# Performance work log

Measured on AMD Instinct MI355X. Metric: run time of the kernel, lower is better.

Reference implementation:

```python
import jax, jax.numpy as jnp
import numpy as np

NUM_EMBEDDINGS = 1024
EMBEDDING_DIM = 256
COMMITMENT_COST = 0.25


def setup_inputs() -> dict:
    key = jax.random.key(0)
    k1, k2 = jax.random.split(key)
    inputs = jax.random.normal(k1, (32, EMBEDDING_DIM, 32, 32), dtype=jnp.float32)
    # codebook init matches torch: uniform(-1/K, 1/K)
    weight = jax.random.uniform(
        k2, (NUM_EMBEDDINGS, EMBEDDING_DIM), dtype=jnp.float32,
        minval=-1.0 / NUM_EMBEDDINGS, maxval=1.0 / NUM_EMBEDDINGS)
    return {"inputs": inputs, "weight": weight}


def reference(inputs, weight):
    # inputs: [B, C, H, W] with C == EMBEDDING_DIM; weight: [K, D]
    x = jnp.transpose(inputs, (0, 2, 3, 1))            # [B, H, W, D]
    input_shape = x.shape
    flat = x.reshape(-1, EMBEDDING_DIM)                # [N, D]

    distances = (jnp.sum(flat * flat, axis=1, keepdims=True)
                 + jnp.sum(weight * weight, axis=1)
                 - 2.0 * (flat @ weight.T))
    encoding_indices = jnp.argmin(distances, axis=1)   # [N]
    encodings = jax.nn.one_hot(encoding_indices, NUM_EMBEDDINGS, dtype=jnp.float32)  # [N, K]

    # one_hot @ weight == gather; use gather for efficiency (same values)
    quantized = weight[encoding_indices].reshape(input_shape)  # [B, H, W, D]

    e_latent_loss = jnp.mean((jax.lax.stop_gradient(quantized) - x) ** 2)
    q_latent_loss = jnp.mean((quantized - jax.lax.stop_gradient(x)) ** 2)
    loss = q_latent_loss + COMMITMENT_COST * e_latent_loss

    # straight-through estimator
    quantized_st = x + jax.lax.stop_gradient(quantized - x)

    avg_probs = jnp.mean(encodings, axis=0)            # [K]
    perplexity = jnp.exp(-jnp.sum(avg_probs * jnp.log(avg_probs + 1e-10)))

    return (loss,
            jnp.transpose(quantized_st, (0, 3, 1, 2)),  # back to [B, C, H, W]
            perplexity,
            encodings)
```

## Files before the change

### kernel.cpp

```cpp
#include <hip/hip_runtime.h>
#include <hip/hip_bf16.h>

#define HWDIM 1024
#define DDIM 256
#define KCODES 1024
#define NROWS 32768
#define BSTRIDE (DDIM * HWDIM)
#define GUARD 1.5e-4f

typedef __attribute__((ext_vector_type(8))) short short8;
typedef __attribute__((ext_vector_type(4))) float f32x4;
typedef unsigned long long ull;


__device__ __forceinline__ unsigned short f2bf(float v) {
  __hip_bfloat16 b = __float2bfloat16(v);
  return *reinterpret_cast<unsigned short*>(&b);
}
__device__ __forceinline__ float bf2f(unsigned short u) {
  __hip_bfloat16 b;
  *reinterpret_cast<unsigned short*>(&b) = u;
  return __bfloat162float(b);
}
__device__ __forceinline__ ull pk(float d, int k) {
  unsigned ub = __float_as_uint(d);
  ub = (ub & 0x80000000u) ? ~ub : (ub | 0x80000000u);
  return ((ull)ub << 32) | (unsigned)k;
}
__device__ __forceinline__ float keyq(ull key) {
  unsigned ub = (unsigned)(key >> 32);
  unsigned orig = (ub & 0x80000000u) ? (ub & 0x7FFFFFFFu) : ~ub;
  return __uint_as_float(orig);
}

__device__ __forceinline__ float pair128_sq(const float* p, int stride) {
  float a[8];
#pragma unroll
  for (int j = 0; j < 8; ++j) { float v = p[j * stride]; a[j] = __fmul_rn(v, v); }
  for (int i = 8; i < 128; i += 8) {
#pragma unroll
    for (int j = 0; j < 8; ++j) {
      float v = p[(i + j) * stride];
      a[j] = __fadd_rn(a[j], __fmul_rn(v, v));
    }
  }
  float s01 = __fadd_rn(a[0], a[1]), s23 = __fadd_rn(a[2], a[3]);
  float s45 = __fadd_rn(a[4], a[5]), s67 = __fadd_rn(a[6], a[7]);
  return __fadd_rn(__fadd_rn(s01, s23), __fadd_rn(s45, s67));
}

__global__ __launch_bounds__(256) void k_prep(
    const float* __restrict__ w, float* __restrict__ wT, float* __restrict__ ss,
    int* __restrict__ hist, double* __restrict__ loss, int* __restrict__ wcount,
    unsigned short* __restrict__ wh8, unsigned short* __restrict__ wl8) {
  __shared__ float tile[64][65];
  const int t = threadIdx.x;
  int g = blockIdx.x * 256 + t;
  {
    int k = g >> 5, oct = g & 31;
    const float* p = w + k * DDIM + oct * 8;
    short8 hv, lv;
#pragma unroll
    for (int j = 0; j < 8; ++j) {
      float v = p[j];
      unsigned short h = f2bf(v);
      unsigned short l = f2bf(__fsub_rn(v, bf2f(h)));
      hv[j] = (short)h; lv[j] = (short)l;
    }
    *(short8*)&wh8[oct * 8192 + k * 8] = hv;
    *(short8*)&wl8[oct * 8192 + k * 8] = lv;
  }
  if (g < KCODES) {
    hist[g] = 0;
    const float* p = w + g * DDIM;
    ss[g] = __fadd_rn(pair128_sq(p, 1), pair128_sq(p + 128, 1));
  }
  if (g == 0) { *loss = 0.0; *wcount = 0; }
  if (blockIdx.x < 64) {
    const int k0 = (blockIdx.x & 15) * 64, d0 = (blockIdx.x >> 4) * 64;
    const int c = t & 63, r = t >> 6;
#pragma unroll
    for (int m = 0; m < 16; ++m)
      tile[r + m * 4][c] = w[(k0 + r + m * 4) * DDIM + d0 + c];
    __syncthreads();
#pragma unroll
    for (int m = 0; m < 16; ++m)
      wT[(size_t)(d0 + r + m * 4) * KCODES + k0 + c] = tile[c][r + m * 4];
  }
}

__global__ __launch_bounds__(256) void k_argmfma(
    const float* __restrict__ in,
    const unsigned short* __restrict__ wh8, const unsigned short* __restrict__ wl8,
    const float* __restrict__ ss, unsigned* __restrict__ kkarr,
    int* __restrict__ wlist, int* __restrict__ wcount) {
  __shared__ __align__(16) unsigned short Ah[32 * 64 * 8];
  __shared__ __align__(16) unsigned short Al[32 * 64 * 8];
  __shared__ ull best1[64], best2[64];

  const int t = threadIdx.x;
  const int n0 = blockIdx.x * 64;
  const int b = n0 >> 10, hw0 = n0 & 1023;

  {
    const int hw = t & 63, dg = t >> 6;
    const float* xp = in + b * BSTRIDE + hw0 + hw;
#pragma unroll
    for (int dd = 0; dd < 64; dd += 2) {
      int d = dg * 64 + dd;
      float f0 = xp[d * HWDIM], f1 = xp[(d + 1) * HWDIM];
      unsigned short h0 = f2bf(f0);
      unsigned short l0 = f2bf(__fsub_rn(f0, bf2f(h0)));
      unsigned short h1 = f2bf(f1);
      unsigned short l1 = f2bf(__fsub_rn(f1, bf2f(h1)));
      int base = ((d >> 3) * 64 + hw) * 8 + (d & 7);
      *(unsigned*)&Ah[base] = (unsigned)h0 | ((unsigned)h1 << 16);
      *(unsigned*)&Al[base] = (unsigned)l0 | ((unsigned)l1 << 16);
    }
  }
  if (t < 64) { best1[t] = ~0ull; best2[t] = ~0ull; }
  __syncthreads();

  const int wv = t >> 6, ln = t & 63;
  const int rw = (wv & 1) * 32;
  const int cw = (wv >> 1) * 64;
  const int l15 = ln & 15, quad = ln >> 4;

  ull rb1[8], rb2[8];
#pragma unroll
  for (int i = 0; i < 8; ++i) { rb1[i] = ~0ull; rb2[i] = ~0ull; }

  for (int kb = 0; kb < 8; ++kb) {
    const int cb = kb * 128 + cw;
    f32x4 acc[2][4];
#pragma unroll
    for (int rt = 0; rt < 2; ++rt)
#pragma unroll
      for (int ct = 0; ct < 4; ++ct) acc[rt][ct] = (f32x4){0.f, 0.f, 0.f, 0.f};

#pragma unroll
    for (int ki = 0; ki < 8; ++ki) {
      const int obase = ki * 4 + quad;
      short8 ah[2], al[2], bh[4], bl[4];
#pragma unroll
      for (int rt = 0; rt < 2; ++rt) {
        int row = rw + rt * 16 + l15;
        ah[rt] = *(const short8*)&Ah[(obase * 64 + row) * 8];
        al[rt] = *(const short8*)&Al[(obase * 64 + row) * 8];
      }
#pragma unroll
      for (int ct = 0; ct < 4; ++ct) {
        int off = obase * 8192 + (cb + ct * 16 + l15) * 8;
        bh[ct] = *(const short8*)&wh8[off];
        bl[ct] = *(const short8*)&wl8[off];
      }
#pragma unroll
      for (int rt = 0; rt < 2; ++rt)
#pragma unroll
        for (int ct = 0; ct < 4; ++ct) {
          acc[rt][ct] = __builtin_amdgcn_mfma_f32_16x16x32_bf16(ah[rt], bh[ct], acc[rt][ct], 0, 0, 0);
          acc[rt][ct] = __builtin_amdgcn_mfma_f32_16x16x32_bf16(ah[rt], bl[ct], acc[rt][ct], 0, 0, 0);
          acc[rt][ct] = __builtin_amdgcn_mfma_f32_16x16x32_bf16(al[rt], bh[ct], acc[rt][ct], 0, 0, 0);
        }
    }

    float sv[4];
#pragma unroll
    for (int ct = 0; ct < 4; ++ct) sv[ct] = ss[cb + ct * 16 + l15];
#pragma unroll
    for (int rt = 0; rt < 2; ++rt)
#pragma unroll
      for (int reg = 0; reg < 4; ++reg) {
        int idx = rt * 4 + reg;
        ull b1 = rb1[idx], b2 = rb2[idx];
#pragma unroll
        for (int ct = 0; ct < 4; ++ct) {
          float q = fmaf(-2.f, acc[rt][ct][reg], sv[ct]);
          ull key = pk(q, cb + ct * 16 + l15);
          if (key < b1) { b2 = b1; b1 = key; } else if (key < b2) { b2 = key; }
        }
        rb1[idx] = b1; rb2[idx] = b2;
      }
  }

#pragma unroll
  for (int rt = 0; rt < 2; ++rt)
#pragma unroll
    for (int reg = 0; reg < 4; ++reg)
      atomicMin(&best1[rw + rt * 16 + quad * 4 + reg], rb1[rt * 4 + reg]);
  __syncthreads();
#pragma unroll
  for (int rt = 0; rt < 2; ++rt)
#pragma unroll
    for (int reg = 0; reg < 4; ++reg) {
      int row = rw + rt * 16 + quad * 4 + reg;
      int idx = rt * 4 + reg;
      ull sub = (rb1[idx] == best1[row]) ? rb2[idx] : rb1[idx];
      atomicMin(&best2[row], sub);
    }
  __syncthreads();
  if (t < 64) {
    ull k1 = best1[t];
    kkarr[n0 + t] = (unsigned)(k1 & 0xFFFFFFFFull);
    if (!(keyq(best2[t]) - keyq(k1) > GUARD)) {
      int p = atomicAdd(wcount, 1);
      wlist[p] = n0 + t;
    }
  }
}

__global__ __launch_bounds__(256) void k_zero(float* __restrict__ e) {
  const size_t tid = (size_t)blockIdx.x * 256 + threadIdx.x;
  float4* p4 = reinterpret_cast<float4*>(e + 2);
  const float4 z = make_float4(0.f, 0.f, 0.f, 0.f);
  const size_t stride = (size_t)gridDim.x * 256;
  for (size_t i = tid; i < 8388607ull; i += stride) p4[i] = z;
  if (tid == 0) { e[0] = 0.f; e[1] = 0.f; e[33554430] = 0.f; e[33554431] = 0.f; }
}

__global__ __launch_bounds__(256) void k_fallback(
    const float* __restrict__ in, const float* __restrict__ wT,
    const float* __restrict__ ss, const int* __restrict__ wlist,
    const int* __restrict__ wcount, unsigned* __restrict__ kkarr) {
  __shared__ float xrow[256];
  __shared__ float rsh;
  __shared__ ull bmin;
  const int t = threadIdx.x;
  const int cnt = *wcount;
  for (int i = blockIdx.x; i < cnt; i += gridDim.x) {
    const int n = wlist[i];
    const int b = n >> 10, hw = n & 1023;
    xrow[t] = in[b * BSTRIDE + t * HWDIM + hw];
    if (t == 0) bmin = ~0ull;
    __syncthreads();
    if (t == 0) rsh = __fadd_rn(pair128_sq(xrow, 1), pair128_sq(xrow + 128, 1));
    __syncthreads();
    float m[4] = {0.f, 0.f, 0.f, 0.f};
    for (int d = 0; d < 256; ++d) {
      float xv = xrow[d];
      const float* wd = wT + (size_t)d * KCODES + t;
      m[0] = fmaf(xv, wd[0], m[0]);
      m[1] = fmaf(xv, wd[256], m[1]);
      m[2] = fmaf(xv, wd[512], m[2]);
      m[3] = fmaf(xv, wd[768], m[3]);
    }
    ull lb = ~0ull;
#pragma unroll
    for (int j = 0; j < 4; ++j) {
      int k = t + j * 256;
      float dist = fmaf(-2.f, m[j], __fadd_rn(rsh, ss[k]));
      ull key = pk(dist, k);
      if (key < lb) lb = key;
    }
    atomicMin(&bmin, lb);
    __syncthreads();
    if (t == 0) kkarr[n] = (unsigned)(bmin & 0xFFFFFFFFull);
    __syncthreads();
  }
}

__global__ __launch_bounds__(256) void k_quant(
    const float* __restrict__ in, const float* __restrict__ w,
    const unsigned* __restrict__ kkarr, int* __restrict__ hist,
    float* __restrict__ enc, float* __restrict__ outq, double* __restrict__ loss) {
  __shared__ float wrow[64][65];
  __shared__ unsigned kk[64];
  __shared__ double red[256];

  const int t = threadIdx.x;
  const int n0 = (blockIdx.x >> 2) * 64;
  const int dc = (blockIdx.x & 3) * 64;
  const int b = n0 >> 10, hw0 = n0 & 1023;

  if (t < 64) kk[t] = kkarr[n0 + t];
  __syncthreads();

  if (dc == 0 && t < 64) {
    unsigned k = kk[t];
    atomicAdd(&hist[k], 1);
    enc[(size_t)(n0 + t) * 1024 + k] = 1.0f;
  }

#pragma unroll
  for (int m = 0; m < 16; ++m) {
    int u = t + m * 256;
    int r = u >> 6, dd = u & 63;
    wrow[r][dd] = w[kk[r] * DDIM + dc + dd];
  }
  __syncthreads();

  const float* inb = in + b * BSTRIDE + hw0;
  float* outb = outq + b * BSTRIDE + hw0;
  const int hwl = t & 63, dl = t >> 6;
  double lsum = 0.0;
#pragma unroll
  for (int dd = 0; dd < 64; dd += 4) {
    int d = dc + dd + dl;
    float x = inb[d * HWDIM + hwl];
    float wv = wrow[hwl][dd + dl];
    float diff = __fsub_rn(wv, x);
    outb[d * HWDIM + hwl] = __fadd_rn(x, diff);
    lsum += (double)diff * (double)diff;
  }
  red[t] = lsum;
  __syncthreads();
  for (int s = 128; s > 0; s >>= 1) {
    if (t < s) red[t] += red[t + s];
    __syncthreads();
  }
  if (t == 0) atomicAdd(loss, red[0]);
}

__global__ void k_final(const int* __restrict__ hist, const double* __restrict__ loss,
                        float* __restrict__ out) {
  __shared__ double red[256];
  int t = threadIdx.x;
  double s = 0.0;
  for (int i = t; i < KCODES; i += 256) {
    double p = (double)hist[i] * (1.0 / 32768.0);
    s += p * log(p + 1e-10);
  }
  red[t] = s;
  __syncthreads();
  for (int st = 128; st > 0; st >>= 1) {
    if (t < st) red[t] += red[t + st];
    __syncthreads();
  }
  if (t == 0) {
    out[8388609] = (float)exp(-red[0]);
    double m = *loss / 8388608.0;
    out[0] = (float)(1.25 * m);
  }
}

extern "C" void kernel_launch(void* const* d_in, const int* in_sizes, int n_in,
                              void* d_out, int out_size, void* d_ws, size_t ws_size,
                              hipStream_t stream) {
  const float* in = (const float*)d_in[0];
  const float* w  = (const float*)d_in[1];
  float* out = (float*)d_out;

  char* wsb = (char*)d_ws;
  float*    wT     = (float*)   (wsb + 0);
  float*    ssp    = (float*)   (wsb + 1048576);
  unsigned* kkarr  = (unsigned*)(wsb + 1052672);
  int*      wlist  = (int*)     (wsb + 1183744);
  int*      hist   = (int*)     (wsb + 1314816);
  int*      wcount = (int*)     (wsb + 1318912);
  double*   loss   = (double*)  (wsb + 1449984);

  char* ob = (char*)d_out + 33554448;
  unsigned short* wh8 = (unsigned short*)(ob + 0);
  unsigned short* wl8 = (unsigned short*)(ob + 524288);
  float* encp = out + 8388610;

  k_prep<<<dim3(128), dim3(256), 0, stream>>>(w, wT, ssp, hist, loss, wcount, wh8, wl8);
  k_argmfma<<<dim3(512), dim3(256), 0, stream>>>(in, wh8, wl8, ssp, kkarr, wlist, wcount);
  k_zero<<<dim3(2048), dim3(256), 0, stream>>>(encp);
  k_fallback<<<dim3(1024), dim3(256), 0, stream>>>(in, wT, ssp, wlist, wcount, kkarr);
  k_quant<<<dim3(2048), dim3(256), 0, stream>>>(in, w, kkarr, hist, encp, out + 1, loss);
  k_final<<<dim3(1), dim3(256), 0, stream>>>(hist, loss, out);
}
```

Measured before the change: 357.3 us.

## Track top-3 candidates to cheapen fallback and fuse one-hot zeroing into quant

The argmin kernel now keeps a third-best candidate per row. Rows whose top two are close but whose third is clearly separated are sent to a cheap two-candidate exact recheck instead of the full 1024-code fallback. Separately, the separate zeroing kernel for the one-hot encodings is removed, and the quant kernel writes full encoding rows (zeros plus the one) with float2 stores. This removes a full pass over the 128 MB encoding buffer and most fallback dot products, at the cost of extra register pressure and compare logic in the MFMA kernel.

```diff
diff --git a/kernel.cpp b/kernel.cpp
--- a/kernel.cpp
+++ b/kernel.cpp
@@ -51,7 +51,8 @@
 
 __global__ __launch_bounds__(256) void k_prep(
     const float* __restrict__ w, float* __restrict__ wT, float* __restrict__ ss,
-    int* __restrict__ hist, double* __restrict__ loss, int* __restrict__ wcount,
+    int* __restrict__ hist, double* __restrict__ loss,
+    int* __restrict__ wcount, int* __restrict__ pcount,
     unsigned short* __restrict__ wh8, unsigned short* __restrict__ wl8) {
   __shared__ float tile[64][65];
   const int t = threadIdx.x;
@@ -75,7 +76,7 @@
     const float* p = w + g * DDIM;
     ss[g] = __fadd_rn(pair128_sq(p, 1), pair128_sq(p + 128, 1));
   }
-  if (g == 0) { *loss = 0.0; *wcount = 0; }
+  if (g == 0) { *loss = 0.0; *wcount = 0; *pcount = 0; }
   if (blockIdx.x < 64) {
     const int k0 = (blockIdx.x & 15) * 64, d0 = (blockIdx.x >> 4) * 64;
     const int c = t & 63, r = t >> 6;
@@ -93,10 +94,11 @@
     const float* __restrict__ in,
     const unsigned short* __restrict__ wh8, const unsigned short* __restrict__ wl8,
     const float* __restrict__ ss, unsigned* __restrict__ kkarr,
-    int* __restrict__ wlist, int* __restrict__ wcount) {
+    int* __restrict__ wlist, int* __restrict__ wcount,
+    int* __restrict__ plist, int* __restrict__ pcount) {
   __shared__ __align__(16) unsigned short Ah[32 * 64 * 8];
   __shared__ __align__(16) unsigned short Al[32 * 64 * 8];
-  __shared__ ull best1[64], best2[64];
+  __shared__ ull best1[64], best2[64], best3[64];
 
   const int t = threadIdx.x;
   const int n0 = blockIdx.x * 64;
@@ -118,7 +120,7 @@
       *(unsigned*)&Al[base] = (unsigned)l0 | ((unsigned)l1 << 16);
     }
   }
-  if (t < 64) { best1[t] = ~0ull; best2[t] = ~0ull; }
+  if (t < 64) { best1[t] = ~0ull; best2[t] = ~0ull; best3[t] = ~0ull; }
   __syncthreads();
 
   const int wv = t >> 6, ln = t & 63;
@@ -126,9 +128,9 @@
   const int cw = (wv >> 1) * 64;
   const int l15 = ln & 15, quad = ln >> 4;
 
-  ull rb1[8], rb2[8];
-#pragma unroll
-  for (int i = 0; i < 8; ++i) { rb1[i] = ~0ull; rb2[i] = ~0ull; }
+  ull rb1[8], rb2[8], rb3[8];
+#pragma unroll
+  for (int i = 0; i < 8; ++i) { rb1[i] = ~0ull; rb2[i] = ~0ull; rb3[i] = ~0ull; }
 
   for (int kb = 0; kb < 8; ++kb) {
     const int cb = kb * 128 + cw;
@@ -172,14 +174,16 @@
 #pragma unroll
       for (int reg = 0; reg < 4; ++reg) {
         int idx = rt * 4 + reg;
-        ull b1 = rb1[idx], b2 = rb2[idx];
+        ull b1 = rb1[idx], b2 = rb2[idx], b3 = rb3[idx];
 #pragma unroll
         for (int ct = 0; ct < 4; ++ct) {
           float q = fmaf(-2.f, acc[rt][ct][reg], sv[ct]);
           ull key = pk(q, cb + ct * 16 + l15);
-          if (key < b1) { b2 = b1; b1 = key; } else if (key < b2) { b2 = key; }
+          if (key < b1)      { b3 = b2; b2 = b1; b1 = key; }
+          else if (key < b2) { b3 = b2; b2 = key; }
+          else if (key < b3) { b3 = key; }
         }
-        rb1[idx] = b1; rb2[idx] = b2;
+        rb1[idx] = b1; rb2[idx] = b2; rb3[idx] = b3;
       }
   }
 
@@ -199,33 +203,73 @@
       atomicMin(&best2[row], sub);
     }
   __syncthreads();
+#pragma unroll
+  for (int rt = 0; rt < 2; ++rt)
+#pragma unroll
+    for (int reg = 0; reg < 4; ++reg) {
+      int row = rw + rt * 16 + quad * 4 + reg;
+      int idx = rt * 4 + reg;
+      ull b1 = best1[row], b2 = best2[row];
+      ull c = (rb1[idx] != b1 && rb1[idx] != b2) ? rb1[idx]
+            : ((rb2[idx] != b1 && rb2[idx] != b2) ? rb2[idx] : rb3[idx]);
+      atomicMin(&best3[row], c);
+    }
+  __syncthreads();
   if (t < 64) {
     ull k1 = best1[t];
     kkarr[n0 + t] = (unsigned)(k1 & 0xFFFFFFFFull);
-    if (!(keyq(best2[t]) - keyq(k1) > GUARD)) {
-      int p = atomicAdd(wcount, 1);
-      wlist[p] = n0 + t;
-    }
-  }
-}
-
-__global__ __launch_bounds__(256) void k_zero(float* __restrict__ e) {
-  const size_t tid = (size_t)blockIdx.x * 256 + threadIdx.x;
-  float4* p4 = reinterpret_cast<float4*>(e + 2);
-  const float4 z = make_float4(0.f, 0.f, 0.f, 0.f);
-  const size_t stride = (size_t)gridDim.x * 256;
-  for (size_t i = tid; i < 8388607ull; i += stride) p4[i] = z;
-  if (tid == 0) { e[0] = 0.f; e[1] = 0.f; e[33554430] = 0.f; e[33554431] = 0.f; }
+    float q1 = keyq(k1);
+    if (!(keyq(best2[t]) - q1 > GUARD)) {
+      if (keyq(best3[t]) - q1 > GUARD) {
+        int p = atomicAdd(pcount, 1);
+        plist[p] = (n0 + t) | ((int)(best2[t] & 0xFFFFFFFFull) << 16);
+      } else {
+        int p = atomicAdd(wcount, 1);
+        wlist[p] = n0 + t;
+      }
+    }
+  }
 }
 
 __global__ __launch_bounds__(256) void k_fallback(
-    const float* __restrict__ in, const float* __restrict__ wT,
-    const float* __restrict__ ss, const int* __restrict__ wlist,
-    const int* __restrict__ wcount, unsigned* __restrict__ kkarr) {
+    const float* __restrict__ in, const float* __restrict__ w,
+    const float* __restrict__ wT, const float* __restrict__ ss,
+    const int* __restrict__ wlist, const int* __restrict__ wcount,
+    const int* __restrict__ plist, const int* __restrict__ pcount,
+    unsigned* __restrict__ kkarr) {
   __shared__ float xrow[256];
   __shared__ float rsh;
   __shared__ ull bmin;
+  __shared__ ull pkeys[2];
   const int t = threadIdx.x;
+
+  const int pc = *pcount;
+  for (int i = blockIdx.x; i < pc; i += gridDim.x) {
+    const int pe = plist[i];
+    const int n = pe & 0xFFFF;
+    const unsigned k2 = ((unsigned)pe) >> 16;
+    const unsigned k1 = kkarr[n];
+    const int b = n >> 10, hw = n & 1023;
+    xrow[t] = in[b * BSTRIDE + t * HWDIM + hw];
+    __syncthreads();
+    if (t == 0) rsh = __fadd_rn(pair128_sq(xrow, 1), pair128_sq(xrow + 128, 1));
+    __syncthreads();
+    if (t < 2) {
+      unsigned k = t ? k2 : k1;
+      const float* wr = w + (size_t)k * DDIM;
+      float m = 0.f;
+      for (int d = 0; d < 256; ++d) m = fmaf(xrow[d], wr[d], m);
+      float dist = fmaf(-2.f, m, __fadd_rn(rsh, ss[k]));
+      pkeys[t] = pk(dist, (int)k);
+    }
+    __syncthreads();
+    if (t == 0) {
+      ull kmin = pkeys[0] < pkeys[1] ? pkeys[0] : pkeys[1];
+      kkarr[n] = (unsigned)(kmin & 0xFFFFFFFFull);
+    }
+    __syncthreads();
+  }
+
   const int cnt = *wcount;
   for (int i = blockIdx.x; i < cnt; i += gridDim.x) {
     const int n = wlist[i];
@@ -259,7 +303,7 @@
   }
 }
 
-__global__ __launch_bounds__(256) void k_quant(
+__global__ __launch_bounds__(256) void k_quantenc(
     const float* __restrict__ in, const float* __restrict__ w,
     const unsigned* __restrict__ kkarr, int* __restrict__ hist,
     float* __restrict__ enc, float* __restrict__ outq, double* __restrict__ loss) {
@@ -268,17 +312,27 @@
   __shared__ double red[256];
 
   const int t = threadIdx.x;
+  const int q = blockIdx.x & 3;
   const int n0 = (blockIdx.x >> 2) * 64;
-  const int dc = (blockIdx.x & 3) * 64;
+  const int dc = q * 64;
+  const int c0 = q * 256;
   const int b = n0 >> 10, hw0 = n0 & 1023;
 
   if (t < 64) kk[t] = kkarr[n0 + t];
   __syncthreads();
 
-  if (dc == 0 && t < 64) {
-    unsigned k = kk[t];
-    atomicAdd(&hist[k], 1);
-    enc[(size_t)(n0 + t) * 1024 + k] = 1.0f;
+  if (q == 0 && t < 64) atomicAdd(&hist[kk[t]], 1);
+
+#pragma unroll 4
+  for (int m = 0; m < 32; ++m) {
+    int u = m * 256 + t;
+    int r = u >> 7, c2 = u & 127;
+    int cbase = c0 + c2 * 2;
+    unsigned kr = kk[r];
+    float2 v;
+    v.x = (cbase == (int)kr) ? 1.0f : 0.0f;
+    v.y = (cbase + 1 == (int)kr) ? 1.0f : 0.0f;
+    *(float2*)&enc[(size_t)(n0 + r) * 1024 + cbase] = v;
   }
 
 #pragma unroll
@@ -346,18 +400,22 @@
   unsigned* kkarr  = (unsigned*)(wsb + 1052672);
   int*      wlist  = (int*)     (wsb + 1183744);
   int*      hist   = (int*)     (wsb + 1314816);
-  int*      wcount = (int*)     (wsb + 1318912);
+  int*      plist  = (int*)     (wsb + 1318912);
   double*   loss   = (double*)  (wsb + 1449984);
+  int*      wcount = (int*)     (wsb + 1449992);
+  int*      pcount = (int*)     (wsb + 1449996);
 
   char* ob = (char*)d_out + 33554448;
   unsigned short* wh8 = (unsigned short*)(ob + 0);
   unsigned short* wl8 = (unsigned short*)(ob + 524288);
   float* encp = out + 8388610;
 
-  k_prep<<<dim3(128), dim3(256), 0, stream>>>(w, wT, ssp, hist, loss, wcount, wh8, wl8);
-  k_argmfma<<<dim3(512), dim3(256), 0, stream>>>(in, wh8, wl8, ssp, kkarr, wlist, wcount);
-  k_zero<<<dim3(2048), dim3(256), 0, stream>>>(encp);
-  k_fallback<<<dim3(1024), dim3(256), 0, stream>>>(in, wT, ssp, wlist, wcount, kkarr);
-  k_quant<<<dim3(2048), dim3(256), 0, stream>>>(in, w, kkarr, hist, encp, out + 1, loss);
+  k_prep<<<dim3(128), dim3(256), 0, stream>>>(w, wT, ssp, hist, loss, wcount, pcount, wh8, wl8);
+  k_argmfma<<<dim3(512), dim3(256), 0, stream>>>(in, wh8, wl8, ssp, kkarr,
+                                                 wlist, wcount, plist, pcount);
+  k_fallback<<<dim3(1024), dim3(256), 0, stream>>>(in, w, wT, ssp, wlist, wcount,
+                                                   plist, pcount, kkarr);
+  k_quantenc<<<dim3(2048), dim3(256), 0, stream>>>(in, w, kkarr, hist, encp,
+                                                   out + 1, loss);
   k_final<<<dim3(1), dim3(256), 0, stream>>>(hist, loss, out);
 }
```

Result: faster. 342.1 us (-4.2%).
